# Performance work log

Measured on AMD Instinct MI355X. Metric: run time of the kernel, lower is better.

Reference implementation:

```python
import jax, jax.numpy as jnp
import numpy as np

# Config constants (repo-level globals)
N, S, P = 4096, 64, 64          # total peds, scenes, peds per scene (uniform)
H, E, MLPD, BOT = 64, 16, 64, 32  # h_dim, EMBEDDING_DIM, MLP_DIM, BOTTLENECK_DIM
PRED_LEN = 12
MIN_DIM = 3                      # mlp_input_dim = [rel_pos(2), speed(1)]
PP_HID = 512                     # hidden width of mlp_pre_pool


def setup_inputs() -> dict:
    key = jax.random.key(0)
    ks = jax.random.split(key, 24)
    sc = 0.1
    starts = jnp.arange(S, dtype=jnp.int32) * P
    inp = {
        "last_pos": jax.random.normal(ks[0], (N, 2), jnp.float32),
        "last_pos_rel": jax.random.normal(ks[1], (N, 2), jnp.float32),
        "h0": jax.random.normal(ks[2], (1, N, H), jnp.float32),
        "c0": jax.random.normal(ks[3], (1, N, H), jnp.float32),
        "pred_ped_speed": jax.random.uniform(ks[4], (PRED_LEN, N, 1), jnp.float32),
        # spatial_embedding: Linear(3, E)
        "W_sp": jax.random.normal(ks[5], (MIN_DIM, E)) * sc, "b_sp": jnp.zeros(E),
        # LSTM cell (torch gate order i,f,g,o)
        "W_ih": jax.random.normal(ks[6], (E, 4 * H)) * sc, "b_ih": jnp.zeros(4 * H),
        "W_hh": jax.random.normal(ks[7], (H, 4 * H)) * sc, "b_hh": jnp.zeros(4 * H),
        # hidden2pos: Linear(H, 2)
        "W_h2p": jax.random.normal(ks[8], (H, 2)) * sc, "b_h2p": jnp.zeros(2),
        # pooling pos_embedding: Linear(3, E)
        "W_pe": jax.random.normal(ks[9], (MIN_DIM, E)) * sc, "b_pe": jnp.zeros(E),
        # mlp_pre_pool: [E+H, 512, BOT], relu, no BN
        "W_pp1": jax.random.normal(ks[10], (E + H, PP_HID)) * sc, "b_pp1": jnp.zeros(PP_HID),
        "W_pp2": jax.random.normal(ks[11], (PP_HID, BOT)) * sc, "b_pp2": jnp.zeros(BOT),
        # decoder mlp: [H+BOT, MLPD, H], relu, no BN
        "W_m1": jax.random.normal(ks[12], (H + BOT, MLPD)) * sc, "b_m1": jnp.zeros(MLPD),
        "W_m2": jax.random.normal(ks[13], (MLPD, H)) * sc, "b_m2": jnp.zeros(H),
        "seq_start_end": jnp.stack([starts, starts + P], axis=1),
        "train_or_test": 0,
    }
    return inp


def reference(last_pos, last_pos_rel, h0, c0, pred_ped_speed,
              W_sp, b_sp, W_ih, b_ih, W_hh, b_hh, W_h2p, b_h2p,
              W_pe, b_pe, W_pp1, b_pp1, W_pp2, b_pp2,
              W_m1, b_m1, W_m2, b_m2, seq_start_end, train_or_test):
    relu = jax.nn.relu

    def lstm_cell(x, h, c):
        g = x @ W_ih + b_ih + h @ W_hh + b_hh
        i, f, gg, o = jnp.split(g, 4, axis=-1)
        c = jax.nn.sigmoid(f) * c + jax.nn.sigmoid(i) * jnp.tanh(gg)
        h = jax.nn.sigmoid(o) * jnp.tanh(c)
        return h, c

    def pool(h, pos, spd):
        # uniform scenes: reshape [N,*] -> [S,P,*]; pairwise index [s,i,j]
        hg = h.reshape(S, P, H)
        pg = pos.reshape(S, P, 2)
        sg = spd.reshape(S, P, 1)
        # social feature [s,i,j] = pos[j] - pos[i]  (curr_end_pos_1 - curr_end_pos_2)
        rel = pg[:, None, :, :] - pg[:, :, None, :]              # [S,P,P,2]
        feat = jnp.concatenate(
            [rel, jnp.broadcast_to(sg[:, None, :, :], (S, P, P, 1))], -1)  # speed of j
        emb = feat @ W_pe + b_pe                                  # [S,P,P,E]
        pre = jnp.concatenate(
            [jnp.broadcast_to(hg[:, None, :, :], (S, P, P, H)), emb], -1)  # h of j
        x = relu(pre @ W_pp1 + b_pp1)
        x = relu(x @ W_pp2 + b_pp2)                               # [S,P,P,BOT]
        return x.max(axis=2).reshape(-1, BOT)                     # max over j -> [N,BOT]

    # speed used at step id is pred_ped_speed[id+1], last step reuses final speed
    spd_seq = jnp.concatenate([pred_ped_speed[1:], pred_ped_speed[-1:]], axis=0)
    x0 = jnp.concatenate([last_pos_rel, pred_ped_speed[0]], -1) @ W_sp + b_sp

    def step(carry, spd_t):
        h, c, lp, x = carry
        h, c = lstm_cell(x, h, c)
        rel_pos = h @ W_h2p + b_h2p
        curr = rel_pos + lp
        x_new = jnp.concatenate([rel_pos, spd_t], -1) @ W_sp + b_sp
        pool_h = pool(h, curr, spd_t)
        h_new = relu(relu(jnp.concatenate([h, pool_h], -1) @ W_m1 + b_m1) @ W_m2 + b_m2)
        return (h_new, c, curr, x_new), rel_pos

    carry = (h0[0], c0[0], last_pos, x0)
    _, rels = jax.lax.scan(step, carry, spd_seq)
    return rels  # [PRED_LEN, N, 2]
```

## Files before the change

### kernel.cpp

```cpp
#include <hip/hip_runtime.h>

typedef unsigned int  u32;
typedef unsigned short u16;
typedef float  f32x4 __attribute__((ext_vector_type(4)));
typedef u32    u32x4 __attribute__((ext_vector_type(4)));
typedef __bf16 bf16x8 __attribute__((ext_vector_type(8)));
typedef _Float16 f16;
typedef _Float16 f16x8 __attribute__((ext_vector_type(8)));
typedef _Float16 f16x2 __attribute__((ext_vector_type(2)));

static constexpr int NPED = 4096;
static constexpr int H = 64, E = 16, BOT = 32, PPH = 512;
static constexpr int TSTEPS = 12;

__device__ __forceinline__ float bf2f(u16 u) {
  return __builtin_bit_cast(float, ((u32)u) << 16);
}
__device__ __forceinline__ u16 f2bf(float f) {
  u32 u = __builtin_bit_cast(u32, f);
  u += 0x7fffu + ((u >> 16) & 1u);
  return (u16)(u >> 16);
}
__device__ __forceinline__ u16 f2h(float f) {
  return __builtin_bit_cast(u16, (f16)f);
}
__device__ __forceinline__ float sigm(float x) { return 1.f / (1.f + __expf(-x)); }
__device__ __forceinline__ float tanhf_(float x) {
  float t = fabsf(x);
  float e = __expf(-2.f * t);
  float r = (1.f - e) / (1.f + e);
  return x < 0.f ? -r : r;
}
__device__ __forceinline__ f16x8 relu8(f16x8 t) {
  const f16x8 z = {(f16)0, (f16)0, (f16)0, (f16)0, (f16)0, (f16)0, (f16)0, (f16)0};
#if __has_builtin(__builtin_elementwise_max)
  return __builtin_elementwise_max(t, z);
#else
  #pragma unroll
  for (int q = 0; q < 8; ++q) t[q] = t[q] > (f16)0 ? t[q] : (f16)0;
  return t;
#endif
}

__device__ __forceinline__ void gload_lds16(const u16* __restrict__ g, u16* l) {
#if __has_builtin(__builtin_amdgcn_global_load_lds)
  __builtin_amdgcn_global_load_lds(
      (const __attribute__((address_space(1))) void*)g,
      (__attribute__((address_space(3))) void*)l, 16, 0, 0);
#else
  *(u32x4*)l = *(const u32x4*)g;
#endif
}

static constexpr size_t OFF_C    = 0;
static constexpr size_t OFF_HL   = 1048576;
static constexpr size_t OFF_POS  = 2097152;
static constexpr size_t OFF_X    = 2129920;
static constexpr size_t OFF_POOL = 2392064;
static constexpr size_t OFF_ABF  = 2916352;
static constexpr size_t OFF_A3   = 7110656;
static constexpr size_t OFF_CST  = 7116800;
static constexpr size_t OFF_W2T  = 7118848;
static constexpr size_t OFF_GWH  = 7151616;
static constexpr size_t OFF_GWL  = 7200768;
static constexpr size_t OFF_D1H  = 7249920;
static constexpr size_t OFF_D1L  = 7262208;
static constexpr size_t OFF_D2H  = 7274496;
static constexpr size_t OFF_D2L  = 7282688;
static constexpr size_t OFF_PWH  = 7290880;
static constexpr size_t OFF_PWL  = 7356416;
static constexpr size_t OFF_ABF2 = 7421952;
static constexpr size_t ABF_BYTES = (size_t)NPED * PPH * 2;
static constexpr size_t WS_NEED_FUSED = OFF_ABF2 + ABF_BYTES;

static constexpr int POOL_SMEM = 64*520*2 + 32*520*2 + 16*512*2 + 16*4*2*16*4;
static constexpr int FUSED_SMEM = POOL_SMEM + 64 + 128 + 128;

__global__ void k_setup(const float* __restrict__ last_pos, const float* __restrict__ last_pos_rel,
                        const float* __restrict__ c0, const float* __restrict__ pps,
                        const float* __restrict__ W_sp, const float* __restrict__ b_sp,
                        const float* __restrict__ W_pe, const float* __restrict__ b_pe,
                        const float* __restrict__ W_pp1, const float* __restrict__ b_pp1,
                        const float* __restrict__ W_pp2,
                        const float* __restrict__ W_ih, const float* __restrict__ W_hh,
                        const float* __restrict__ W_m1, const float* __restrict__ W_m2,
                        float* __restrict__ c, float* __restrict__ pos, float* __restrict__ x,
                        float* __restrict__ A3, float* __restrict__ Cst, u16* __restrict__ W2t,
                        u16* GWH, u16* GWL, u16* D1H, u16* D1L,
                        u16* D2H, u16* D2L, u16* PWH, u16* PWL)
{
  const int stride = gridDim.x * blockDim.x;
  const int tid0 = blockIdx.x * blockDim.x + threadIdx.x;
  for (int i = tid0; i < NPED * H; i += stride) c[i] = c0[i];
  for (int i = tid0; i < NPED * 2; i += stride) pos[i] = last_pos[i];
  for (int i = tid0; i < NPED * E; i += stride) {
    int n = i >> 4, e = i & 15;
    x[i] = last_pos_rel[2*n] * W_sp[e] + last_pos_rel[2*n+1] * W_sp[16+e]
         + pps[n] * W_sp[32+e] + b_sp[e];
  }
  for (int i = tid0; i < 3 * PPH; i += stride) {
    int r = i >> 9, k = i & 511;
    float s = 0.f;
    for (int e = 0; e < 16; ++e) s += W_pe[r*16+e] * W_pp1[(64+e)*PPH + k];
    A3[i] = s;
  }
  for (int i = tid0; i < PPH; i += stride) {
    float s = b_pp1[i];
    for (int e = 0; e < 16; ++e) s += b_pe[e] * W_pp1[(64+e)*PPH + i];
    Cst[i] = s;
  }
  for (int i = tid0; i < 32 * PPH; i += stride) {
    int n = i >> 9, k = i & 511;
    W2t[i] = f2h(W_pp2[k*32 + n]);
  }
  for (int i = tid0; i < 256*96; i += stride) {
    int n = i / 96, k = i - n*96;
    float wv = (k < 16) ? W_ih[k*256+n] : ((k < 80) ? W_hh[(k-16)*256+n] : 0.f);
    u16 hi = f2bf(wv); u16 lo = f2bf(wv - bf2f(hi));
    int idx = (((n>>4)*3 + (k>>5))*64 + ((k>>3)&3)*16 + (n&15))*8 + (k&7);
    GWH[idx] = hi; GWL[idx] = lo;
  }
  for (int i = tid0; i < 64*96; i += stride) {
    int n = i / 96, k = i - n*96;
    float wv = W_m1[k*64 + n];
    u16 hi = f2bf(wv); u16 lo = f2bf(wv - bf2f(hi));
    int idx = (((n>>4)*3 + (k>>5))*64 + ((k>>3)&3)*16 + (n&15))*8 + (k&7);
    D1H[idx] = hi; D1L[idx] = lo;
  }
  for (int i = tid0; i < 64*64; i += stride) {
    int n = i >> 6, k = i & 63;
    float wv = W_m2[k*64 + n];
    u16 hi = f2bf(wv); u16 lo = f2bf(wv - bf2f(hi));
    int idx = (((n>>4)*2 + (k>>5))*64 + ((k>>3)&3)*16 + (n&15))*8 + (k&7);
    D2H[idx] = hi; D2L[idx] = lo;
  }
  for (int i = tid0; i < 512*64; i += stride) {
    int n = i >> 6, k = i & 63;
    float wv = W_pp1[k*PPH + n];
    u16 hi = f2bf(wv); u16 lo = f2bf(wv - bf2f(hi));
    int idx = (((n>>4)*2 + (k>>5))*64 + ((k>>3)&3)*16 + (n&15))*8 + (k&7);
    PWH[idx] = hi; PWL[idx] = lo;
  }
}

template<int NT, int NKS>
__device__ __forceinline__ void load_frags(const u16* __restrict__ WH, const u16* __restrict__ WL,
                                           int tile0, int lane,
                                           u32x4 (&bh)[NT][NKS], u32x4 (&bl)[NT][NKS])
{
  #pragma unroll
  for (int i = 0; i < NT; ++i)
    #pragma unroll
    for (int ks = 0; ks < NKS; ++ks) {
      int o = (((tile0 + i)*NKS + ks)*64 + lane)*8;
      bh[i][ks] = *(const u32x4*)(WH + o);
      bl[i][ks] = *(const u32x4*)(WL + o);
    }
}

template<int NT, int NKS>
__device__ __forceinline__ void mfma_compute(const u32x4 (&bh)[NT][NKS], const u32x4 (&bl)[NT][NKS],
                                             int lane, const float* arow, f32x4* acc)
{
  const int kg = lane >> 4;
  #pragma unroll
  for (int ks = 0; ks < NKS; ++ks) {
    f32x4 a0 = *(const f32x4*)(arow + ks*32 + kg*8);
    f32x4 a1 = *(const f32x4*)(arow + ks*32 + kg*8 + 4);
    float av[8] = {a0.x,a0.y,a0.z,a0.w,a1.x,a1.y,a1.z,a1.w};
    bf16x8 ah, al;
    #pragma unroll
    for (int j = 0; j < 8; ++j) {
      __bf16 hbits = (__bf16)av[j];
      ah[j] = hbits;
      al[j] = (__bf16)(av[j] - (float)hbits);
    }
    #pragma unroll
    for (int i = 0; i < NT; ++i) {
      bf16x8 BH = __builtin_bit_cast(bf16x8, bh[i][ks]);
      bf16x8 BL = __builtin_bit_cast(bf16x8, bl[i][ks]);
      acc[i] = __builtin_amdgcn_mfma_f32_16x16x32_bf16(ah, BH, acc[i], 0, 0, 0);
      acc[i] = __builtin_amdgcn_mfma_f32_16x16x32_bf16(ah, BL, acc[i], 0, 0, 0);
      acc[i] = __builtin_amdgcn_mfma_f32_16x16x32_bf16(al, BH, acc[i], 0, 0, 0);
    }
  }
}

template<int NT, int NKS>
__device__ __forceinline__ void mfma_block(
    const u16* __restrict__ WH, const u16* __restrict__ WL, int tile0, int lane,
    const float* arow, int acol0, f32x4* acc)
{
  u32x4 bh[NT][NKS], bl[NT][NKS];
  load_frags<NT,NKS>(WH, WL, tile0, lane, bh, bl);
  mfma_compute<NT,NKS>(bh, bl, lane, arow + acol0, acc);
}

__global__ __launch_bounds__(256) void k_step(
    int t,
    const float* __restrict__ h0, const float* __restrict__ pps,
    float* __restrict__ c, float* __restrict__ h_lstm,
    float* __restrict__ pos, float* __restrict__ x, const float* __restrict__ pool,
    const float* __restrict__ b_ih, const float* __restrict__ b_hh,
    const float* __restrict__ W_h2p, const float* __restrict__ b_h2p,
    const float* __restrict__ W_sp, const float* __restrict__ b_sp,
    const float* __restrict__ b_m1, const float* __restrict__ b_m2,
    const float* __restrict__ A3, const float* __restrict__ Cst,
    const u16* __restrict__ GWH, const u16* __restrict__ GWL,
    const u16* __restrict__ D1H, const u16* __restrict__ D1L,
    const u16* __restrict__ D2H, const u16* __restrict__ D2L,
    const u16* __restrict__ PWH, const u16* __restrict__ PWL,
    u16* __restrict__ a_bf, float* __restrict__ out)
{
  __shared__ float zin[16][100];
  __shared__ float o1[16][68];
  __shared__ float as_[16][100];
  __shared__ float hl[16][68];
  __shared__ float gl[16][260];
  __shared__ float rel_s[16][2], pos_s[16][2], spd_s[16];

  const int tid = threadIdx.x;
  const int p0 = blockIdx.x * 16;
  const int w = tid >> 6, lane = tid & 63, colq = lane & 15, kg = lane >> 4;
  const int tsp = (t + 1 < 12) ? t + 1 : 11;

  { int p = tid >> 4, e = tid & 15;
    as_[p][e] = x[(p0 + p) * E + e];
    as_[p][80 + e] = 0.f; }
  if (tid < 16) spd_s[tid] = pps[tsp * NPED + p0 + tid];
  if (t == 0) {
    #pragma unroll
    for (int q = 0; q < 4; ++q) {
      int idx = tid + 256*q; int p = idx >> 6, d = idx & 63;
      as_[p][16 + d] = h0[(p0 + p) * H + d];
    }
  } else {
    #pragma unroll
    for (int q = 0; q < 4; ++q) {
      int idx = tid + 256*q; int p = idx >> 6, d = idx & 63;
      zin[p][d] = h_lstm[(p0 + p) * H + d];
    }
    #pragma unroll
    for (int q = 0; q < 2; ++q) {
      int idx = tid + 256*q; int p = idx >> 5, d = idx & 31;
      zin[p][64 + d] = pool[(p0 + p) * BOT + d];
    }
  }
  __syncthreads();

  if (t > 0) {
    {
      f32x4 acc = {0.f, 0.f, 0.f, 0.f};
      mfma_block<1,3>(D1H, D1L, w, lane, &zin[colq][0], 0, &acc);
      int n = w*16 + colq;
      float bm = b_m1[n];
      #pragma unroll
      for (int r = 0; r < 4; ++r) o1[kg*4 + r][n] = fmaxf(acc[r] + bm, 0.f);
    }
    __syncthreads();
    {
      f32x4 acc = {0.f, 0.f, 0.f, 0.f};
      mfma_block<1,2>(D2H, D2L, w, lane, &o1[colq][0], 0, &acc);
      int n = w*16 + colq;
      float bm = b_m2[n];
      #pragma unroll
      for (int r = 0; r < 4; ++r) as_[kg*4 + r][16 + n] = fmaxf(acc[r] + bm, 0.f);
    }
    __syncthreads();
  }

  {
    f32x4 gacc[4];
    #pragma unroll
    for (int i = 0; i < 4; ++i) gacc[i] = (f32x4){0.f,0.f,0.f,0.f};
    mfma_block<2,3>(GWH, GWL, w*4,     lane, &as_[colq][0], 0, &gacc[0]);
    mfma_block<2,3>(GWH, GWL, w*4 + 2, lane, &as_[colq][0], 0, &gacc[2]);
    #pragma unroll
    for (int i = 0; i < 4; ++i) {
      int n = (w*4 + i)*16 + colq;
      float bb = b_ih[n] + b_hh[n];
      #pragma unroll
      for (int r = 0; r < 4; ++r) gl[kg*4 + r][n] = gacc[i][r] + bb;
    }
  }
  __syncthreads();

  #pragma unroll
  for (int q = 0; q < 4; ++q) {
    int idx = tid + 256*q; int p = idx >> 6, d = idx & 63; int n = p0 + p;
    float gi = gl[p][d], gf = gl[p][64 + d], gg = gl[p][128 + d], go = gl[p][192 + d];
    float cv = c[n*H + d];
    float cn = sigm(gf) * cv + sigm(gi) * tanhf_(gg);
    float hv = sigm(go) * tanhf_(cn);
    c[n*H + d] = cn;
    hl[p][d] = hv;
    h_lstm[n*H + d] = hv;
  }
  __syncthreads();

  {
    int p = tid >> 4, l = tid & 15;
    f32x4 hv = *(const f32x4*)(&hl[p][0] + l*4);
    float s0 = hv.x * W_h2p[(l*4+0)*2]   + hv.y * W_h2p[(l*4+1)*2]
             + hv.z * W_h2p[(l*4+2)*2]   + hv.w * W_h2p[(l*4+3)*2];
    float s1 = hv.x * W_h2p[(l*4+0)*2+1] + hv.y * W_h2p[(l*4+1)*2+1]
             + hv.z * W_h2p[(l*4+2)*2+1] + hv.w * W_h2p[(l*4+3)*2+1];
    #pragma unroll
    for (int m = 1; m < 16; m <<= 1) {
      s0 += __shfl_xor(s0, m, 64);
      s1 += __shfl_xor(s1, m, 64);
    }
    if (l == 0) {
      float r0 = s0 + b_h2p[0], r1 = s1 + b_h2p[1];
      int n = p0 + p;
      float px = pos[n*2] + r0, py = pos[n*2+1] + r1;
      pos[n*2] = px; pos[n*2+1] = py;
      rel_s[p][0] = r0; rel_s[p][1] = r1;
      pos_s[p][0] = px; pos_s[p][1] = py;
      out[(t*NPED + n)*2] = r0; out[(t*NPED + n)*2 + 1] = r1;
    }
  }
  __syncthreads();

  if (t < 11) {
    {
      int p = tid >> 4, e = tid & 15;
      float xv = rel_s[p][0] * W_sp[e] + rel_s[p][1] * W_sp[16+e]
               + spd_s[p] * W_sp[32+e] + b_sp[e];
      x[(p0 + p) * E + e] = xv;
    }
    {
      f32x4 pacc[8];
      #pragma unroll
      for (int i = 0; i < 8; ++i) pacc[i] = (f32x4){0.f,0.f,0.f,0.f};
      mfma_block<4,2>(PWH, PWL, w*8,     lane, &hl[colq][0], 0, &pacc[0]);
      mfma_block<4,2>(PWH, PWL, w*8 + 4, lane, &hl[colq][0], 0, &pacc[4]);
      #pragma unroll
      for (int i = 0; i < 8; ++i) {
        int n = (w*8 + i)*16 + colq;
        float a3x = A3[n], a3y = A3[512 + n], a3s = A3[1024 + n], cst = Cst[n];
        #pragma unroll
        for (int r = 0; r < 4; ++r) {
          int p2 = kg*4 + r;
          float val = pacc[i][r] + pos_s[p2][0]*a3x + pos_s[p2][1]*a3y
                    + spd_s[p2]*a3s + cst;
          a_bf[(size_t)(p0 + p2)*PPH + n] = f2h(val);
        }
      }
    }
  }
}

__global__ __launch_bounds__(1024) void k_pool(
    const u16* __restrict__ a_bf, const float* __restrict__ pos,
    const float* __restrict__ A3, const u16* __restrict__ W2t,
    const float* __restrict__ b_pp2, float* __restrict__ pool)
{
  constexpr int LDA = 520;
  extern __shared__ char smem_raw[];
  u16* a_s  = (u16*)smem_raw;
  u16* w2_s = a_s + 64 * LDA;
  f16* v_s  = (f16*)(w2_s + 32 * LDA);
  float* red = (float*)(v_s + 16 * 512);

  const int tid = threadIdx.x;
  const int s = blockIdx.y;
  const int i0 = blockIdx.x * 16;

  for (int idx = tid; idx < 4096; idx += 1024) {
    int r = idx >> 6, c8 = (idx & 63) * 8;
    *(u32x4*)&a_s[r * LDA + c8] = *(const u32x4*)&a_bf[(s * 64 + r) * PPH + c8];
  }
  for (int idx = tid; idx < 2048; idx += 1024) {
    int r = idx >> 6, c8 = (idx & 63) * 8;
    *(u32x4*)&w2_s[r * LDA + c8] = *(const u32x4*)&W2t[r * PPH + c8];
  }
  for (int idx = tid; idx < 4096; idx += 1024) {
    int i = idx >> 8, k2 = (idx & 255) * 2;
    int n = s * 64 + i0 + i;
    float px = pos[n * 2], py = pos[n * 2 + 1];
    float v0 = px * A3[k2]     + py * A3[512 + k2];
    float v1 = px * A3[k2 + 1] + py * A3[512 + k2 + 1];
    f16x2 pk = { (f16)v0, (f16)v1 };
    *(f16x2*)&v_s[i * 512 + k2] = pk;
  }
  __syncthreads();

  const int lane = tid & 63, w = tid >> 6;
  const int jq = w & 3, g = w >> 2;
  const int col = lane & 15, kg = lane >> 4;
  const int aoff  = (jq * 16 + col) * LDA + kg * 8;
  const int w0off = col * LDA + kg * 8;
  const int w1off = (col + 16) * LDA + kg * 8;
  const float b20 = b_pp2[col];
  const float b21 = b_pp2[col + 16];
  const f32x4 vzero = {0.f, 0.f, 0.f, 0.f};

  f32x4 accA[4], accB[4];
  #pragma unroll
  for (int ii = 0; ii < 4; ++ii) { accA[ii] = vzero; accB[ii] = vzero; }

  for (int kk = 0; kk < 16; ++kk) {
    const int ke = kk * 32;
    f16x8 a8  = __builtin_bit_cast(f16x8, *(const u32x4*)&a_s[aoff + ke]);
    f16x8 bw0 = __builtin_bit_cast(f16x8, *(const u32x4*)&w2_s[w0off + ke]);
    f16x8 bw1 = __builtin_bit_cast(f16x8, *(const u32x4*)&w2_s[w1off + ke]);
    #pragma unroll
    for (int ii = 0; ii < 4; ++ii) {
      f16x8 v8 = *(const f16x8*)&v_s[(g * 4 + ii) * 512 + ke + kg * 8];
      f16x8 tq = relu8(a8 - v8);
      accA[ii] = __builtin_amdgcn_mfma_f32_16x16x32_f16(tq, bw0, accA[ii], 0, 0, 0);
      accB[ii] = __builtin_amdgcn_mfma_f32_16x16x32_f16(tq, bw1, accB[ii], 0, 0, 0);
    }
  }

  #pragma unroll
  for (int ii = 0; ii < 4; ++ii) {
    float m0 = 0.f, m1 = 0.f;
    #pragma unroll
    for (int r = 0; r < 4; ++r) {
      m0 = fmaxf(m0, accA[ii][r] + b20);
      m1 = fmaxf(m1, accB[ii][r] + b21);
    }
    m0 = fmaxf(m0, __shfl_xor(m0, 16, 64));
    m0 = fmaxf(m0, __shfl_xor(m0, 32, 64));
    m1 = fmaxf(m1, __shfl_xor(m1, 16, 64));
    m1 = fmaxf(m1, __shfl_xor(m1, 32, 64));
    if (kg == 0) {
      red[((w * 4 + ii) * 2 + 0) * 16 + col] = m0;
      red[((w * 4 + ii) * 2 + 1) * 16 + col] = m1;
    }
  }
  __syncthreads();

  if (tid < 512) {
    int gg = tid >> 7, ii = (tid >> 5) & 3, tile = (tid >> 4) & 1, cc = tid & 15;
    float m = red[(((gg * 4 + 0) * 4 + ii) * 2 + tile) * 16 + cc];
    #pragma unroll
    for (int q = 1; q < 4; ++q)
      m = fmaxf(m, red[(((gg * 4 + q) * 4 + ii) * 2 + tile) * 16 + cc]);
    int i = i0 + gg * 4 + ii;
    pool[(s * 64 + i) * 32 + tile * 16 + cc] = m;
  }
}

__global__ __launch_bounds__(1024) void k_fused(
    int t,
    const float* __restrict__ h0, const float* __restrict__ pps,
    float* __restrict__ c, float* __restrict__ h_lstm,
    float* __restrict__ pos, float* __restrict__ x,
    const float* __restrict__ b_ih, const float* __restrict__ b_hh,
    const float* __restrict__ W_h2p, const float* __restrict__ b_h2p,
    const float* __restrict__ W_sp, const float* __restrict__ b_sp,
    const float* __restrict__ b_m1, const float* __restrict__ b_m2,
    const float* __restrict__ A3, const float* __restrict__ Cst,
    const u16* __restrict__ GWH, const u16* __restrict__ GWL,
    const u16* __restrict__ D1H, const u16* __restrict__ D1L,
    const u16* __restrict__ D2H, const u16* __restrict__ D2L,
    const u16* __restrict__ PWH, const u16* __restrict__ PWL,
    const u16* __restrict__ W2t, const float* __restrict__ b_pp2,
    const u16* __restrict__ a_read, u16* __restrict__ a_write,
    float* __restrict__ out)
{
  constexpr int LDA = 520;
  extern __shared__ char smem_raw[];
  u16*   a_s    = (u16*)smem_raw;
  u16*   w2_s   = a_s + 64 * LDA;
  f16*   v_s    = (f16*)(w2_s + 32 * LDA);
  float* red    = (float*)(v_s + 16 * 512);
  float* spd_s  = red + 16*4*2*16;
  float* rel_s  = spd_s + 16;
  float* pos_s  = rel_s + 32;
  float* zin = (float*)smem_raw;
  float* o1  = zin + 16*100;
  float* as_ = o1  + 16*68;
  float* hl  = as_ + 16*100;
  float* gl  = hl  + 16*68;

  const int tid = threadIdx.x;
  const int s = blockIdx.y;
  const int i0 = blockIdx.x * 16;
  const int p0 = s * 64 + i0;
  const int lane = tid & 63, w = tid >> 6;
  const int colq = lane & 15, kg = lane >> 4;
  const int sd = tid & 63;
  const int tsp = (t + 1 < 12) ? t + 1 : 11;

  const float* hsrc = (t == 0) ? h0 : h_lstm;
  float hreg = hsrc[(p0 + w) * H + sd];
  float creg = c[(p0 + w) * H + sd];
  float whp0 = W_h2p[2 * sd], whp1 = W_h2p[2 * sd + 1];
  float xreg = 0.f;
  if (tid < 256) xreg = x[(p0 + (tid >> 4)) * E + (tid & 15)];
  if (tid < 16) spd_s[tid] = pps[tsp * NPED + p0 + tid];

  u32x4 gh[1][3], glo[1][3];
  u32x4 d1h_[1][3], d1l_[1][3], d2h_[1][2], d2l_[1][2];

  if (t > 0) {
    #pragma unroll
    for (int q = 0; q < 4; ++q) {
      int r = w + 16 * q;
      gload_lds16(&a_read[(size_t)(s * 64 + r) * PPH + lane * 8],
                  &a_s[r * LDA + lane * 8]);
    }
    #pragma unroll
    for (int q = 0; q < 2; ++q) {
      int r = w + 16 * q;
      gload_lds16(&W2t[(size_t)r * PPH + lane * 8],
                  &w2_s[r * LDA + lane * 8]);
    }
    for (int idx = tid; idx < 4096; idx += 1024) {
      int i = idx >> 8, k2 = (idx & 255) * 2;
      int n = s * 64 + i0 + i;
      float px = pos[n * 2], py = pos[n * 2 + 1];
      float v0 = px * A3[k2]     + py * A3[512 + k2];
      float v1 = px * A3[k2 + 1] + py * A3[512 + k2 + 1];
      f16x2 pk = { (f16)v0, (f16)v1 };
      *(f16x2*)&v_s[i * 512 + k2] = pk;
    }
    __syncthreads();

    {
      const int jq = w & 3, g = w >> 2;
      const int aoff  = (jq * 16 + colq) * LDA + kg * 8;
      const int w0off = colq * LDA + kg * 8;
      const int w1off = (colq + 16) * LDA + kg * 8;
      const float b20 = b_pp2[colq];
      const float b21 = b_pp2[colq + 16];
      const f32x4 vzero = {0.f, 0.f, 0.f, 0.f};

      f32x4 accA[4], accB[4];
      #pragma unroll
      for (int ii = 0; ii < 4; ++ii) { accA[ii] = vzero; accB[ii] = vzero; }

      for (int kk = 0; kk < 16; ++kk) {
        const int ke = kk * 32;
        f16x8 a8  = __builtin_bit_cast(f16x8, *(const u32x4*)&a_s[aoff + ke]);
        f16x8 bw0 = __builtin_bit_cast(f16x8, *(const u32x4*)&w2_s[w0off + ke]);
        f16x8 bw1 = __builtin_bit_cast(f16x8, *(const u32x4*)&w2_s[w1off + ke]);
        #pragma unroll
        for (int ii = 0; ii < 4; ++ii) {
          f16x8 v8 = *(const f16x8*)&v_s[(g * 4 + ii) * 512 + ke + kg * 8];
          f16x8 tq = relu8(a8 - v8);
          accA[ii] = __builtin_amdgcn_mfma_f32_16x16x32_f16(tq, bw0, accA[ii], 0, 0, 0);
          accB[ii] = __builtin_amdgcn_mfma_f32_16x16x32_f16(tq, bw1, accB[ii], 0, 0, 0);
        }
      }

      #pragma unroll
      for (int ii = 0; ii < 4; ++ii) {
        float m0 = 0.f, m1 = 0.f;
        #pragma unroll
        for (int r = 0; r < 4; ++r) {
          m0 = fmaxf(m0, accA[ii][r] + b20);
          m1 = fmaxf(m1, accB[ii][r] + b21);
        }
        m0 = fmaxf(m0, __shfl_xor(m0, 16, 64));
        m0 = fmaxf(m0, __shfl_xor(m0, 32, 64));
        m1 = fmaxf(m1, __shfl_xor(m1, 16, 64));
        m1 = fmaxf(m1, __shfl_xor(m1, 32, 64));
        if (kg == 0) {
          red[((w * 4 + ii) * 2 + 0) * 16 + colq] = m0;
          red[((w * 4 + ii) * 2 + 1) * 16 + colq] = m1;
        }
      }
    }
    load_frags<1,3>(GWH, GWL, w, lane, gh, glo);
    if (w < 4) {
      load_frags<1,3>(D1H, D1L, w, lane, d1h_, d1l_);
      load_frags<1,2>(D2H, D2L, w, lane, d2h_, d2l_);
    }
    __syncthreads();

    zin[w * 100 + sd] = hreg;
    if (tid < 512) {
      int gg = tid >> 7, ii = (tid >> 5) & 3, tile = (tid >> 4) & 1, cc = tid & 15;
      float m = red[(((gg * 4 + 0) * 4 + ii) * 2 + tile) * 16 + cc];
      #pragma unroll
      for (int q = 1; q < 4; ++q)
        m = fmaxf(m, red[(((gg * 4 + q) * 4 + ii) * 2 + tile) * 16 + cc]);
      zin[(gg * 4 + ii) * 100 + 64 + tile * 16 + cc] = m;
    }
    if (tid < 256) { int p = tid >> 4, e = tid & 15;
                     as_[p * 100 + e] = xreg; as_[p * 100 + 80 + e] = 0.f; }
    __syncthreads();

    if (w < 4) {
      f32x4 acc = {0.f, 0.f, 0.f, 0.f};
      mfma_compute<1,3>(d1h_, d1l_, lane, &zin[colq * 100], &acc);
      int n = w * 16 + colq;
      float bm = b_m1[n];
      #pragma unroll
      for (int r = 0; r < 4; ++r) o1[(kg * 4 + r) * 68 + n] = fmaxf(acc[r] + bm, 0.f);
    }
    __syncthreads();

    if (w < 4) {
      f32x4 acc = {0.f, 0.f, 0.f, 0.f};
      mfma_compute<1,2>(d2h_, d2l_, lane, &o1[colq * 68], &acc);
      int n = w * 16 + colq;
      float bm = b_m2[n];
      #pragma unroll
      for (int r = 0; r < 4; ++r) as_[(kg * 4 + r) * 100 + 16 + n] = fmaxf(acc[r] + bm, 0.f);
    }
    __syncthreads();
  } else {
    load_frags<1,3>(GWH, GWL, w, lane, gh, glo);
    as_[w * 100 + 16 + sd] = hreg;
    if (tid < 256) { int p = tid >> 4, e = tid & 15;
                     as_[p * 100 + e] = xreg; as_[p * 100 + 80 + e] = 0.f; }
    __syncthreads();
  }

  {
    f32x4 acc = {0.f, 0.f, 0.f, 0.f};
    mfma_compute<1,3>(gh, glo, lane, &as_[colq * 100], &acc);
    int n = w * 16 + colq;
    float bb = b_ih[n] + b_hh[n];
    #pragma unroll
    for (int r = 0; r < 4; ++r) gl[(kg * 4 + r) * 260 + n] = acc[r] + bb;
  }
  u32x4 ph[2][2], pl[2][2];
  if (t < 11) load_frags<2,2>(PWH, PWL, w * 2, lane, ph, pl);
  __syncthreads();

  {
    int n = p0 + w;
    float gi = gl[w*260 + sd], gf = gl[w*260 + 64 + sd],
          gg = gl[w*260 + 128 + sd], go = gl[w*260 + 192 + sd];
    float cn = sigm(gf) * creg + sigm(gi) * tanhf_(gg);
    float hv = sigm(go) * tanhf_(cn);
    c[n*H + sd] = cn;
    hl[w*68 + sd] = hv;
    h_lstm[n*H + sd] = hv;
    float s0 = hv * whp0, s1 = hv * whp1;
    #pragma unroll
    for (int m = 1; m < 64; m <<= 1) {
      s0 += __shfl_xor(s0, m, 64);
      s1 += __shfl_xor(s1, m, 64);
    }
    if (sd == 0) {
      float r0 = s0 + b_h2p[0], r1 = s1 + b_h2p[1];
      float px = pos[n*2] + r0, py = pos[n*2+1] + r1;
      pos[n*2] = px; pos[n*2+1] = py;
      rel_s[w*2+0] = r0; rel_s[w*2+1] = r1;
      pos_s[w*2+0] = px; pos_s[w*2+1] = py;
      out[(t*NPED + n)*2] = r0; out[(t*NPED + n)*2 + 1] = r1;
    }
  }
  __syncthreads();

  if (t < 11) {
    if (tid < 256) {
      int p = tid >> 4, e = tid & 15;
      float xv = rel_s[p*2+0] * W_sp[e] + rel_s[p*2+1] * W_sp[16+e]
               + spd_s[p] * W_sp[32+e] + b_sp[e];
      x[(p0 + p) * E + e] = xv;
    }
    {
      f32x4 pacc[2];
      pacc[0] = (f32x4){0.f,0.f,0.f,0.f};
      pacc[1] = (f32x4){0.f,0.f,0.f,0.f};
      mfma_compute<2,2>(ph, pl, lane, &hl[colq * 68], pacc);
      #pragma unroll
      for (int i = 0; i < 2; ++i) {
        int n = (w * 2 + i) * 16 + colq;
        float a3x = A3[n], a3y = A3[512 + n], a3s = A3[1024 + n], cst = Cst[n];
        #pragma unroll
        for (int r = 0; r < 4; ++r) {
          int p2 = kg * 4 + r;
          float val = pacc[i][r] + pos_s[p2*2+0]*a3x + pos_s[p2*2+1]*a3y
                    + spd_s[p2]*a3s + cst;
          a_write[(size_t)(p0 + p2) * PPH + n] = f2h(val);
        }
      }
    }
  }
}

extern "C" void kernel_launch(void* const* d_in, const int* in_sizes, int n_in,
                              void* d_out, int out_size, void* d_ws, size_t ws_size,
                              hipStream_t stream)
{
  const float* last_pos     = (const float*)d_in[0];
  const float* last_pos_rel = (const float*)d_in[1];
  const float* h0    = (const float*)d_in[2];
  const float* c0    = (const float*)d_in[3];
  const float* pps   = (const float*)d_in[4];
  const float* W_sp  = (const float*)d_in[5];
  const float* b_sp  = (const float*)d_in[6];
  const float* W_ih  = (const float*)d_in[7];
  const float* b_ih  = (const float*)d_in[8];
  const float* W_hh  = (const float*)d_in[9];
  const float* b_hh  = (const float*)d_in[10];
  const float* W_h2p = (const float*)d_in[11];
  const float* b_h2p = (const float*)d_in[12];
  const float* W_pe  = (const float*)d_in[13];
  const float* b_pe  = (const float*)d_in[14];
  const float* W_pp1 = (const float*)d_in[15];
  const float* b_pp1 = (const float*)d_in[16];
  const float* W_pp2 = (const float*)d_in[17];
  const float* b_pp2 = (const float*)d_in[18];
  const float* W_m1  = (const float*)d_in[19];
  const float* b_m1  = (const float*)d_in[20];
  const float* W_m2  = (const float*)d_in[21];
  const float* b_m2  = (const float*)d_in[22];

  char* ws = (char*)d_ws;
  float* c_buf  = (float*)(ws + OFF_C);
  float* h_lstm = (float*)(ws + OFF_HL);
  float* pos    = (float*)(ws + OFF_POS);
  float* x_buf  = (float*)(ws + OFF_X);
  float* pool   = (float*)(ws + OFF_POOL);
  u16*   abuf0  = (u16*)(ws + OFF_ABF);
  float* A3     = (float*)(ws + OFF_A3);
  float* Cst    = (float*)(ws + OFF_CST);
  u16*   W2t    = (u16*)(ws + OFF_W2T);
  u16* GWH = (u16*)(ws + OFF_GWH); u16* GWL = (u16*)(ws + OFF_GWL);
  u16* D1H = (u16*)(ws + OFF_D1H); u16* D1L = (u16*)(ws + OFF_D1L);
  u16* D2H = (u16*)(ws + OFF_D2H); u16* D2L = (u16*)(ws + OFF_D2L);
  u16* PWH = (u16*)(ws + OFF_PWH); u16* PWL = (u16*)(ws + OFF_PWL);
  u16*   abuf1  = (u16*)(ws + OFF_ABF2);
  float* out    = (float*)d_out;

  const bool fused_ok = (ws_size >= WS_NEED_FUSED);

  hipFuncSetAttribute(reinterpret_cast<const void*>(k_pool),
                      hipFuncAttributeMaxDynamicSharedMemorySize, POOL_SMEM);
  hipFuncSetAttribute(reinterpret_cast<const void*>(k_fused),
                      hipFuncAttributeMaxDynamicSharedMemorySize, FUSED_SMEM);

  k_setup<<<512, 256, 0, stream>>>(last_pos, last_pos_rel, c0, pps, W_sp, b_sp,
                                   W_pe, b_pe, W_pp1, b_pp1, W_pp2,
                                   W_ih, W_hh, W_m1, W_m2,
                                   c_buf, pos, x_buf, A3, Cst, W2t,
                                   GWH, GWL, D1H, D1L, D2H, D2L, PWH, PWL);

  if (fused_ok) {
    for (int t = 0; t < TSTEPS; ++t) {
      const u16* ar = (t > 0 && ((t - 1) & 1)) ? abuf1 : abuf0;
      u16*       aw = (t & 1) ? abuf1 : abuf0;
      k_fused<<<dim3(4, 64), 1024, FUSED_SMEM, stream>>>(
          t, h0, pps, c_buf, h_lstm, pos, x_buf,
          b_ih, b_hh, W_h2p, b_h2p, W_sp, b_sp, b_m1, b_m2, A3, Cst,
          GWH, GWL, D1H, D1L, D2H, D2L, PWH, PWL,
          W2t, b_pp2, ar, aw, out);
    }
  } else {
    k_step<<<256, 256, 0, stream>>>(0, h0, pps, c_buf, h_lstm, pos, x_buf, pool,
                                    b_ih, b_hh, W_h2p, b_h2p, W_sp, b_sp,
                                    b_m1, b_m2, A3, Cst,
                                    GWH, GWL, D1H, D1L, D2H, D2L, PWH, PWL,
                                    abuf0, out);
    for (int t = 1; t < TSTEPS; ++t) {
      k_pool<<<dim3(4, 64), 1024, POOL_SMEM, stream>>>(abuf0, pos, A3, W2t, b_pp2, pool);
      k_step<<<256, 256, 0, stream>>>(t, h0, pps, c_buf, h_lstm, pos, x_buf, pool,
                                      b_ih, b_hh, W_h2p, b_h2p, W_sp, b_sp,
                                      b_m1, b_m2, A3, Cst,
                                      GWH, GWL, D1H, D1L, D2H, D2L, PWH, PWL,
                                      abuf0, out);
    }
  }
}
```

Before: 266.6 us.

## Replace per-step fused launches with one persistent per-scene kernel

Replaces the twelve per-timestep k_fused launches (256 blocks of 16 peds) with a single persistent k_pers kernel where each of 64 blocks owns a whole scene of 64 peds across all timesteps. It keeps h, c, x and positions in registers and shared memory, which removes the global round-trips and the double-buffered pre-pool activation buffer. Since a scene is self-contained, no grid sync is needed. In exchange only 64 blocks run, so each block processes four times as many pool rows sequentially and far fewer CUs are used.

```diff
diff --git a/kernel.cpp b/kernel.cpp
--- a/kernel.cpp
+++ b/kernel.cpp
@@ -72,9 +72,12 @@
 static constexpr size_t OFF_ABF2 = 7421952;
 static constexpr size_t ABF_BYTES = (size_t)NPED * PPH * 2;
 static constexpr size_t WS_NEED_FUSED = OFF_ABF2 + ABF_BYTES;
+static constexpr size_t WS_NEED_PERS  = OFF_ABF + ABF_BYTES;
 
 static constexpr int POOL_SMEM = 64*520*2 + 32*520*2 + 16*512*2 + 16*4*2*16*4;
 static constexpr int FUSED_SMEM = POOL_SMEM + 64 + 128 + 128;
+static constexpr int PERS_UNION = 152576;
+static constexpr int PERS_SMEM  = PERS_UNION + 64*32*4 + 64*4 + 64*2*4 + 64*2*4;
 
 __global__ void k_setup(const float* __restrict__ last_pos, const float* __restrict__ last_pos_rel,
                         const float* __restrict__ c0, const float* __restrict__ pps,
@@ -194,6 +197,278 @@
   u32x4 bh[NT][NKS], bl[NT][NKS];
   load_frags<NT,NKS>(WH, WL, tile0, lane, bh, bl);
   mfma_compute<NT,NKS>(bh, bl, lane, arow + acol0, acc);
+}
+
+__global__ __launch_bounds__(1024) void k_pers(
+    const float* __restrict__ h0, const float* __restrict__ c0,
+    const float* __restrict__ pps,
+    const float* __restrict__ last_pos, const float* __restrict__ x_g,
+    const float* __restrict__ b_ih, const float* __restrict__ b_hh,
+    const float* __restrict__ W_h2p, const float* __restrict__ b_h2p,
+    const float* __restrict__ W_sp, const float* __restrict__ b_sp,
+    const float* __restrict__ b_m1, const float* __restrict__ b_m2,
+    const float* __restrict__ A3, const float* __restrict__ Cst,
+    const u16* __restrict__ GWH, const u16* __restrict__ GWL,
+    const u16* __restrict__ D1H, const u16* __restrict__ D1L,
+    const u16* __restrict__ D2H, const u16* __restrict__ D2L,
+    const u16* __restrict__ PWH, const u16* __restrict__ PWL,
+    const u16* __restrict__ W2t, const float* __restrict__ b_pp2,
+    u16* __restrict__ a_g, float* __restrict__ out)
+{
+  constexpr int LDA = 520;
+  extern __shared__ char smem[];
+  u16*   a_s  = (u16*)smem;
+  u16*   w2_s = a_s + 64 * LDA;
+  f16*   v_s  = (f16*)(w2_s + 32 * LDA);
+  float* red  = (float*)(v_s + 16 * 512);
+  float* zin = (float*)smem;
+  float* o1  = zin + 64*100;
+  float* as_ = o1  + 64*68;
+  float* hl  = as_ + 64*100;
+  float* gl  = hl  + 64*68;
+  float* pool_out = (float*)(smem + PERS_UNION);
+  float* spd_s    = pool_out + 64*32;
+  float* rel_s    = spd_s + 64;
+  float* pos_s    = rel_s + 128;
+
+  const int tid = threadIdx.x;
+  const int base = blockIdx.x * 64;
+  const int lane = tid & 63, w = tid >> 6;
+  const int colq = lane & 15, kg = lane >> 4;
+  const int sd = lane;
+
+  float creg[4], hreg[4];
+  #pragma unroll
+  for (int q = 0; q < 4; ++q) {
+    int p = w + 16*q;
+    creg[q] = c0[(base + p)*H + sd];
+    hreg[q] = h0[(base + p)*H + sd];
+  }
+  float xreg = x_g[(base + (tid >> 4))*E + (tid & 15)];
+  const float whp0 = W_h2p[2*sd], whp1 = W_h2p[2*sd + 1];
+  if (tid < 64) {
+    pos_s[tid*2+0] = last_pos[(base + tid)*2+0];
+    pos_s[tid*2+1] = last_pos[(base + tid)*2+1];
+  }
+  __syncthreads();
+
+  for (int t = 0; t < TSTEPS; ++t) {
+    const int tsp = (t + 1 < 12) ? t + 1 : 11;
+    if (tid < 64) spd_s[tid] = pps[tsp * NPED + base + tid];
+
+    if (t > 0) {
+      #pragma unroll
+      for (int q = 0; q < 4; ++q) {
+        int r = w + 16*q;
+        gload_lds16(&a_g[(size_t)(base + r)*PPH + lane*8], &a_s[r*LDA + lane*8]);
+      }
+      #pragma unroll
+      for (int q = 0; q < 2; ++q) {
+        int r = w + 16*q;
+        gload_lds16(&W2t[(size_t)r*PPH + lane*8], &w2_s[r*LDA + lane*8]);
+      }
+
+      const int jq = w & 3, g2 = w >> 2;
+      const int aoff  = (jq*16 + colq)*LDA + kg*8;
+      const int w0off = colq*LDA + kg*8;
+      const int w1off = (colq + 16)*LDA + kg*8;
+      const float b20 = b_pp2[colq];
+      const float b21 = b_pp2[colq + 16];
+
+      for (int gg = 0; gg < 4; ++gg) {
+        for (int idx = tid; idx < 4096; idx += 1024) {
+          int il = idx >> 8, k2 = (idx & 255)*2;
+          int i = gg*16 + il;
+          float px = pos_s[i*2], py = pos_s[i*2+1];
+          float v0 = px*A3[k2]     + py*A3[512 + k2];
+          float v1 = px*A3[k2+1]   + py*A3[512 + k2 + 1];
+          f16x2 pk = { (f16)v0, (f16)v1 };
+          *(f16x2*)&v_s[il*512 + k2] = pk;
+        }
+        if (gg > 0 && tid < 512) {
+          int g3 = tid >> 7, ii = (tid >> 5) & 3, tile = (tid >> 4) & 1, cc = tid & 15;
+          float m = red[(((g3*4 + 0)*4 + ii)*2 + tile)*16 + cc];
+          #pragma unroll
+          for (int q = 1; q < 4; ++q)
+            m = fmaxf(m, red[(((g3*4 + q)*4 + ii)*2 + tile)*16 + cc]);
+          pool_out[((gg-1)*16 + g3*4 + ii)*32 + tile*16 + cc] = m;
+        }
+        __syncthreads();
+
+        f32x4 accA[4], accB[4];
+        #pragma unroll
+        for (int ii = 0; ii < 4; ++ii) {
+          accA[ii] = (f32x4){0.f,0.f,0.f,0.f};
+          accB[ii] = (f32x4){0.f,0.f,0.f,0.f};
+        }
+        for (int kk = 0; kk < 16; ++kk) {
+          const int ke = kk * 32;
+          f16x8 a8  = __builtin_bit_cast(f16x8, *(const u32x4*)&a_s[aoff + ke]);
+          f16x8 bw0 = __builtin_bit_cast(f16x8, *(const u32x4*)&w2_s[w0off + ke]);
+          f16x8 bw1 = __builtin_bit_cast(f16x8, *(const u32x4*)&w2_s[w1off + ke]);
+          #pragma unroll
+          for (int ii = 0; ii < 4; ++ii) {
+            f16x8 v8 = *(const f16x8*)&v_s[(g2*4 + ii)*512 + ke + kg*8];
+            f16x8 tq = relu8(a8 - v8);
+            accA[ii] = __builtin_amdgcn_mfma_f32_16x16x32_f16(tq, bw0, accA[ii], 0, 0, 0);
+            accB[ii] = __builtin_amdgcn_mfma_f32_16x16x32_f16(tq, bw1, accB[ii], 0, 0, 0);
+          }
+        }
+        #pragma unroll
+        for (int ii = 0; ii < 4; ++ii) {
+          float m0 = 0.f, m1 = 0.f;
+          #pragma unroll
+          for (int r = 0; r < 4; ++r) {
+            m0 = fmaxf(m0, accA[ii][r] + b20);
+            m1 = fmaxf(m1, accB[ii][r] + b21);
+          }
+          m0 = fmaxf(m0, __shfl_xor(m0, 16, 64));
+          m0 = fmaxf(m0, __shfl_xor(m0, 32, 64));
+          m1 = fmaxf(m1, __shfl_xor(m1, 16, 64));
+          m1 = fmaxf(m1, __shfl_xor(m1, 32, 64));
+          if (kg == 0) {
+            red[((w*4 + ii)*2 + 0)*16 + colq] = m0;
+            red[((w*4 + ii)*2 + 1)*16 + colq] = m1;
+          }
+        }
+        __syncthreads();
+      }
+
+      #pragma unroll
+      for (int q = 0; q < 4; ++q) zin[(w + 16*q)*100 + sd] = hreg[q];
+      if (tid < 512) {
+        int g3 = tid >> 7, ii = (tid >> 5) & 3, tile = (tid >> 4) & 1, cc = tid & 15;
+        float m = red[(((g3*4 + 0)*4 + ii)*2 + tile)*16 + cc];
+        #pragma unroll
+        for (int q = 1; q < 4; ++q)
+          m = fmaxf(m, red[(((g3*4 + q)*4 + ii)*2 + tile)*16 + cc]);
+        pool_out[(48 + g3*4 + ii)*32 + tile*16 + cc] = m;
+      }
+      { int p = tid >> 4, e = tid & 15;
+        as_[p*100 + e] = xreg; as_[p*100 + 80 + e] = 0.f; }
+      __syncthreads();
+      for (int idx = tid; idx < 2048; idx += 1024) {
+        int i = idx >> 5, j = idx & 31;
+        zin[i*100 + 64 + j] = pool_out[i*32 + j];
+      }
+      __syncthreads();
+
+      {
+        const int mt = w >> 2, nt = w & 3;
+        f32x4 acc = {0.f, 0.f, 0.f, 0.f};
+        u32x4 dh[1][3], dl[1][3];
+        load_frags<1,3>(D1H, D1L, nt, lane, dh, dl);
+        mfma_compute<1,3>(dh, dl, lane, &zin[(mt*16 + colq)*100], &acc);
+        int n = nt*16 + colq;
+        float bm = b_m1[n];
+        #pragma unroll
+        for (int r = 0; r < 4; ++r)
+          o1[(mt*16 + kg*4 + r)*68 + n] = fmaxf(acc[r] + bm, 0.f);
+      }
+      __syncthreads();
+
+      {
+        const int mt = w >> 2, nt = w & 3;
+        f32x4 acc = {0.f, 0.f, 0.f, 0.f};
+        u32x4 dh[1][2], dl[1][2];
+        load_frags<1,2>(D2H, D2L, nt, lane, dh, dl);
+        mfma_compute<1,2>(dh, dl, lane, &o1[(mt*16 + colq)*68], &acc);
+        int n = nt*16 + colq;
+        float bm = b_m2[n];
+        #pragma unroll
+        for (int r = 0; r < 4; ++r)
+          as_[(mt*16 + kg*4 + r)*100 + 16 + n] = fmaxf(acc[r] + bm, 0.f);
+      }
+      __syncthreads();
+    } else {
+      #pragma unroll
+      for (int q = 0; q < 4; ++q) as_[(w + 16*q)*100 + 16 + sd] = hreg[q];
+      { int p = tid >> 4, e = tid & 15;
+        as_[p*100 + e] = xreg; as_[p*100 + 80 + e] = 0.f; }
+      __syncthreads();
+    }
+
+    {
+      u32x4 gh[1][3], glo[1][3];
+      load_frags<1,3>(GWH, GWL, w, lane, gh, glo);
+      const int n = w*16 + colq;
+      const float bb = b_ih[n] + b_hh[n];
+      #pragma unroll
+      for (int mt = 0; mt < 4; ++mt) {
+        f32x4 acc = {0.f, 0.f, 0.f, 0.f};
+        mfma_compute<1,3>(gh, glo, lane, &as_[(mt*16 + colq)*100], &acc);
+        #pragma unroll
+        for (int r = 0; r < 4; ++r)
+          gl[(mt*16 + kg*4 + r)*260 + n] = acc[r] + bb;
+      }
+    }
+    __syncthreads();
+
+    {
+      float hv4[4];
+      #pragma unroll
+      for (int q = 0; q < 4; ++q) {
+        int p = w + 16*q;
+        float gi = gl[p*260 + sd], gf = gl[p*260 + 64 + sd],
+              gg = gl[p*260 + 128 + sd], go = gl[p*260 + 192 + sd];
+        float cn = sigm(gf)*creg[q] + sigm(gi)*tanhf_(gg);
+        float hv = sigm(go)*tanhf_(cn);
+        creg[q] = cn; hreg[q] = hv; hv4[q] = hv;
+        hl[p*68 + sd] = hv;
+      }
+      #pragma unroll
+      for (int q = 0; q < 4; ++q) {
+        float s0 = hv4[q]*whp0, s1 = hv4[q]*whp1;
+        #pragma unroll
+        for (int m = 1; m < 64; m <<= 1) {
+          s0 += __shfl_xor(s0, m, 64);
+          s1 += __shfl_xor(s1, m, 64);
+        }
+        if (sd == 0) {
+          int p = w + 16*q;
+          float r0 = s0 + b_h2p[0], r1 = s1 + b_h2p[1];
+          float px = pos_s[p*2+0] + r0, py = pos_s[p*2+1] + r1;
+          pos_s[p*2+0] = px; pos_s[p*2+1] = py;
+          rel_s[p*2+0] = r0; rel_s[p*2+1] = r1;
+          int n = base + p;
+          out[(t*NPED + n)*2] = r0; out[(t*NPED + n)*2 + 1] = r1;
+        }
+      }
+    }
+    __syncthreads();
+
+    if (t < 11) {
+      {
+        int p = tid >> 4, e = tid & 15;
+        xreg = rel_s[p*2+0]*W_sp[e] + rel_s[p*2+1]*W_sp[16+e]
+             + spd_s[p]*W_sp[32+e] + b_sp[e];
+      }
+      {
+        u32x4 ph[2][2], pl[2][2];
+        load_frags<2,2>(PWH, PWL, w*2, lane, ph, pl);
+        #pragma unroll
+        for (int mt = 0; mt < 4; ++mt) {
+          f32x4 pacc[2];
+          pacc[0] = (f32x4){0.f,0.f,0.f,0.f};
+          pacc[1] = (f32x4){0.f,0.f,0.f,0.f};
+          mfma_compute<2,2>(ph, pl, lane, &hl[(mt*16 + colq)*68], pacc);
+          #pragma unroll
+          for (int i = 0; i < 2; ++i) {
+            int n = (w*2 + i)*16 + colq;
+            float a3x = A3[n], a3y = A3[512 + n], a3s = A3[1024 + n], cst = Cst[n];
+            #pragma unroll
+            for (int r = 0; r < 4; ++r) {
+              int p2 = mt*16 + kg*4 + r;
+              float val = pacc[i][r] + pos_s[p2*2+0]*a3x + pos_s[p2*2+1]*a3y
+                        + spd_s[p2]*a3s + cst;
+              a_g[(size_t)(base + p2)*PPH + n] = f2h(val);
+            }
+          }
+        }
+      }
+    }
+    __syncthreads();
+  }
 }
 
 __global__ __launch_bounds__(256) void k_step(
@@ -441,241 +716,6 @@
       m = fmaxf(m, red[(((gg * 4 + q) * 4 + ii) * 2 + tile) * 16 + cc]);
     int i = i0 + gg * 4 + ii;
     pool[(s * 64 + i) * 32 + tile * 16 + cc] = m;
-  }
-}
-
-__global__ __launch_bounds__(1024) void k_fused(
-    int t,
-    const float* __restrict__ h0, const float* __restrict__ pps,
-    float* __restrict__ c, float* __restrict__ h_lstm,
-    float* __restrict__ pos, float* __restrict__ x,
-    const float* __restrict__ b_ih, const float* __restrict__ b_hh,
-    const float* __restrict__ W_h2p, const float* __restrict__ b_h2p,
-    const float* __restrict__ W_sp, const float* __restrict__ b_sp,
-    const float* __restrict__ b_m1, const float* __restrict__ b_m2,
-    const float* __restrict__ A3, const float* __restrict__ Cst,
-    const u16* __restrict__ GWH, const u16* __restrict__ GWL,
-    const u16* __restrict__ D1H, const u16* __restrict__ D1L,
-    const u16* __restrict__ D2H, const u16* __restrict__ D2L,
-    const u16* __restrict__ PWH, const u16* __restrict__ PWL,
-    const u16* __restrict__ W2t, const float* __restrict__ b_pp2,
-    const u16* __restrict__ a_read, u16* __restrict__ a_write,
-    float* __restrict__ out)
-{
-  constexpr int LDA = 520;
-  extern __shared__ char smem_raw[];
-  u16*   a_s    = (u16*)smem_raw;
-  u16*   w2_s   = a_s + 64 * LDA;
-  f16*   v_s    = (f16*)(w2_s + 32 * LDA);
-  float* red    = (float*)(v_s + 16 * 512);
-  float* spd_s  = red + 16*4*2*16;
-  float* rel_s  = spd_s + 16;
-  float* pos_s  = rel_s + 32;
-  float* zin = (float*)smem_raw;
-  float* o1  = zin + 16*100;
-  float* as_ = o1  + 16*68;
-  float* hl  = as_ + 16*100;
-  float* gl  = hl  + 16*68;
-
-  const int tid = threadIdx.x;
-  const int s = blockIdx.y;
-  const int i0 = blockIdx.x * 16;
-  const int p0 = s * 64 + i0;
-  const int lane = tid & 63, w = tid >> 6;
-  const int colq = lane & 15, kg = lane >> 4;
-  const int sd = tid & 63;
-  const int tsp = (t + 1 < 12) ? t + 1 : 11;
-
-  const float* hsrc = (t == 0) ? h0 : h_lstm;
-  float hreg = hsrc[(p0 + w) * H + sd];
-  float creg = c[(p0 + w) * H + sd];
-  float whp0 = W_h2p[2 * sd], whp1 = W_h2p[2 * sd + 1];
-  float xreg = 0.f;
-  if (tid < 256) xreg = x[(p0 + (tid >> 4)) * E + (tid & 15)];
-  if (tid < 16) spd_s[tid] = pps[tsp * NPED + p0 + tid];
-
-  u32x4 gh[1][3], glo[1][3];
-  u32x4 d1h_[1][3], d1l_[1][3], d2h_[1][2], d2l_[1][2];
-
-  if (t > 0) {
-    #pragma unroll
-    for (int q = 0; q < 4; ++q) {
-      int r = w + 16 * q;
-      gload_lds16(&a_read[(size_t)(s * 64 + r) * PPH + lane * 8],
-                  &a_s[r * LDA + lane * 8]);
-    }
-    #pragma unroll
-    for (int q = 0; q < 2; ++q) {
-      int r = w + 16 * q;
-      gload_lds16(&W2t[(size_t)r * PPH + lane * 8],
-                  &w2_s[r * LDA + lane * 8]);
-    }
-    for (int idx = tid; idx < 4096; idx += 1024) {
-      int i = idx >> 8, k2 = (idx & 255) * 2;
-      int n = s * 64 + i0 + i;
-      float px = pos[n * 2], py = pos[n * 2 + 1];
-      float v0 = px * A3[k2]     + py * A3[512 + k2];
-      float v1 = px * A3[k2 + 1] + py * A3[512 + k2 + 1];
-      f16x2 pk = { (f16)v0, (f16)v1 };
-      *(f16x2*)&v_s[i * 512 + k2] = pk;
-    }
-    __syncthreads();
-
-    {
-      const int jq = w & 3, g = w >> 2;
-      const int aoff  = (jq * 16 + colq) * LDA + kg * 8;
-      const int w0off = colq * LDA + kg * 8;
-      const int w1off = (colq + 16) * LDA + kg * 8;
-      const float b20 = b_pp2[colq];
-      const float b21 = b_pp2[colq + 16];
-      const f32x4 vzero = {0.f, 0.f, 0.f, 0.f};
-
-      f32x4 accA[4], accB[4];
-      #pragma unroll
-      for (int ii = 0; ii < 4; ++ii) { accA[ii] = vzero; accB[ii] = vzero; }
-
-      for (int kk = 0; kk < 16; ++kk) {
-        const int ke = kk * 32;
-        f16x8 a8  = __builtin_bit_cast(f16x8, *(const u32x4*)&a_s[aoff + ke]);
-        f16x8 bw0 = __builtin_bit_cast(f16x8, *(const u32x4*)&w2_s[w0off + ke]);
-        f16x8 bw1 = __builtin_bit_cast(f16x8, *(const u32x4*)&w2_s[w1off + ke]);
-        #pragma unroll
-        for (int ii = 0; ii < 4; ++ii) {
-          f16x8 v8 = *(const f16x8*)&v_s[(g * 4 + ii) * 512 + ke + kg * 8];
-          f16x8 tq = relu8(a8 - v8);
-          accA[ii] = __builtin_amdgcn_mfma_f32_16x16x32_f16(tq, bw0, accA[ii], 0, 0, 0);
-          accB[ii] = __builtin_amdgcn_mfma_f32_16x16x32_f16(tq, bw1, accB[ii], 0, 0, 0);
-        }
-      }
-
-      #pragma unroll
-      for (int ii = 0; ii < 4; ++ii) {
-        float m0 = 0.f, m1 = 0.f;
-        #pragma unroll
-        for (int r = 0; r < 4; ++r) {
-          m0 = fmaxf(m0, accA[ii][r] + b20);
-          m1 = fmaxf(m1, accB[ii][r] + b21);
-        }
-        m0 = fmaxf(m0, __shfl_xor(m0, 16, 64));
-        m0 = fmaxf(m0, __shfl_xor(m0, 32, 64));
-        m1 = fmaxf(m1, __shfl_xor(m1, 16, 64));
-        m1 = fmaxf(m1, __shfl_xor(m1, 32, 64));
-        if (kg == 0) {
-          red[((w * 4 + ii) * 2 + 0) * 16 + colq] = m0;
-          red[((w * 4 + ii) * 2 + 1) * 16 + colq] = m1;
-        }
-      }
-    }
-    load_frags<1,3>(GWH, GWL, w, lane, gh, glo);
-    if (w < 4) {
-      load_frags<1,3>(D1H, D1L, w, lane, d1h_, d1l_);
-      load_frags<1,2>(D2H, D2L, w, lane, d2h_, d2l_);
-    }
-    __syncthreads();
-
-    zin[w * 100 + sd] = hreg;
-    if (tid < 512) {
-      int gg = tid >> 7, ii = (tid >> 5) & 3, tile = (tid >> 4) & 1, cc = tid & 15;
-      float m = red[(((gg * 4 + 0) * 4 + ii) * 2 + tile) * 16 + cc];
-      #pragma unroll
-      for (int q = 1; q < 4; ++q)
-        m = fmaxf(m, red[(((gg * 4 + q) * 4 + ii) * 2 + tile) * 16 + cc]);
-      zin[(gg * 4 + ii) * 100 + 64 + tile * 16 + cc] = m;
-    }
-    if (tid < 256) { int p = tid >> 4, e = tid & 15;
-                     as_[p * 100 + e] = xreg; as_[p * 100 + 80 + e] = 0.f; }
-    __syncthreads();
-
-    if (w < 4) {
-      f32x4 acc = {0.f, 0.f, 0.f, 0.f};
-      mfma_compute<1,3>(d1h_, d1l_, lane, &zin[colq * 100], &acc);
-      int n = w * 16 + colq;
-      float bm = b_m1[n];
-      #pragma unroll
-      for (int r = 0; r < 4; ++r) o1[(kg * 4 + r) * 68 + n] = fmaxf(acc[r] + bm, 0.f);
-    }
-    __syncthreads();
-
-    if (w < 4) {
-      f32x4 acc = {0.f, 0.f, 0.f, 0.f};
-      mfma_compute<1,2>(d2h_, d2l_, lane, &o1[colq * 68], &acc);
-      int n = w * 16 + colq;
-      float bm = b_m2[n];
-      #pragma unroll
-      for (int r = 0; r < 4; ++r) as_[(kg * 4 + r) * 100 + 16 + n] = fmaxf(acc[r] + bm, 0.f);
-    }
-    __syncthreads();
-  } else {
-    load_frags<1,3>(GWH, GWL, w, lane, gh, glo);
-    as_[w * 100 + 16 + sd] = hreg;
-    if (tid < 256) { int p = tid >> 4, e = tid & 15;
-                     as_[p * 100 + e] = xreg; as_[p * 100 + 80 + e] = 0.f; }
-    __syncthreads();
-  }
-
-  {
-    f32x4 acc = {0.f, 0.f, 0.f, 0.f};
-    mfma_compute<1,3>(gh, glo, lane, &as_[colq * 100], &acc);
-    int n = w * 16 + colq;
-    float bb = b_ih[n] + b_hh[n];
-    #pragma unroll
-    for (int r = 0; r < 4; ++r) gl[(kg * 4 + r) * 260 + n] = acc[r] + bb;
-  }
-  u32x4 ph[2][2], pl[2][2];
-  if (t < 11) load_frags<2,2>(PWH, PWL, w * 2, lane, ph, pl);
-  __syncthreads();
-
-  {
-    int n = p0 + w;
-    float gi = gl[w*260 + sd], gf = gl[w*260 + 64 + sd],
-          gg = gl[w*260 + 128 + sd], go = gl[w*260 + 192 + sd];
-    float cn = sigm(gf) * creg + sigm(gi) * tanhf_(gg);
-    float hv = sigm(go) * tanhf_(cn);
-    c[n*H + sd] = cn;
-    hl[w*68 + sd] = hv;
-    h_lstm[n*H + sd] = hv;
-    float s0 = hv * whp0, s1 = hv * whp1;
-    #pragma unroll
-    for (int m = 1; m < 64; m <<= 1) {
-      s0 += __shfl_xor(s0, m, 64);
-      s1 += __shfl_xor(s1, m, 64);
-    }
-    if (sd == 0) {
-      float r0 = s0 + b_h2p[0], r1 = s1 + b_h2p[1];
-      float px = pos[n*2] + r0, py = pos[n*2+1] + r1;
-      pos[n*2] = px; pos[n*2+1] = py;
-      rel_s[w*2+0] = r0; rel_s[w*2+1] = r1;
-      pos_s[w*2+0] = px; pos_s[w*2+1] = py;
-      out[(t*NPED + n)*2] = r0; out[(t*NPED + n)*2 + 1] = r1;
-    }
-  }
-  __syncthreads();
-
-  if (t < 11) {
-    if (tid < 256) {
-      int p = tid >> 4, e = tid & 15;
-      float xv = rel_s[p*2+0] * W_sp[e] + rel_s[p*2+1] * W_sp[16+e]
-               + spd_s[p] * W_sp[32+e] + b_sp[e];
-      x[(p0 + p) * E + e] = xv;
-    }
-    {
-      f32x4 pacc[2];
-      pacc[0] = (f32x4){0.f,0.f,0.f,0.f};
-      pacc[1] = (f32x4){0.f,0.f,0.f,0.f};
-      mfma_compute<2,2>(ph, pl, lane, &hl[colq * 68], pacc);
-      #pragma unroll
-      for (int i = 0; i < 2; ++i) {
-        int n = (w * 2 + i) * 16 + colq;
-        float a3x = A3[n], a3y = A3[512 + n], a3s = A3[1024 + n], cst = Cst[n];
-        #pragma unroll
-        for (int r = 0; r < 4; ++r) {
-          int p2 = kg * 4 + r;
-          float val = pacc[i][r] + pos_s[p2*2+0]*a3x + pos_s[p2*2+1]*a3y
-                    + spd_s[p2]*a3s + cst;
-          a_write[(size_t)(p0 + p2) * PPH + n] = f2h(val);
-        }
-      }
-    }
   }
 }
 
@@ -721,15 +761,14 @@
   u16* D1H = (u16*)(ws + OFF_D1H); u16* D1L = (u16*)(ws + OFF_D1L);
   u16* D2H = (u16*)(ws + OFF_D2H); u16* D2L = (u16*)(ws + OFF_D2L);
   u16* PWH = (u16*)(ws + OFF_PWH); u16* PWL = (u16*)(ws + OFF_PWL);
-  u16*   abuf1  = (u16*)(ws + OFF_ABF2);
   float* out    = (float*)d_out;
 
-  const bool fused_ok = (ws_size >= WS_NEED_FUSED);
-
-  hipFuncSetAttribute(reinterpret_cast<const void*>(k_pool),
-                      hipFuncAttributeMaxDynamicSharedMemorySize, POOL_SMEM);
-  hipFuncSetAttribute(reinterpret_cast<const void*>(k_fused),
-                      hipFuncAttributeMaxDynamicSharedMemorySize, FUSED_SMEM);
+  static int pers_ok = -1;
+  if (pers_ok < 0) {
+    hipError_t e = hipFuncSetAttribute(reinterpret_cast<const void*>(k_pers),
+                                       hipFuncAttributeMaxDynamicSharedMemorySize, PERS_SMEM);
+    pers_ok = (e == hipSuccess) ? 1 : 0;
+  }
 
   k_setup<<<512, 256, 0, stream>>>(last_pos, last_pos_rel, c0, pps, W_sp, b_sp,
                                    W_pe, b_pe, W_pp1, b_pp1, W_pp2,
@@ -737,17 +776,15 @@
                                    c_buf, pos, x_buf, A3, Cst, W2t,
                                    GWH, GWL, D1H, D1L, D2H, D2L, PWH, PWL);
 
-  if (fused_ok) {
-    for (int t = 0; t < TSTEPS; ++t) {
-      const u16* ar = (t > 0 && ((t - 1) & 1)) ? abuf1 : abuf0;
-      u16*       aw = (t & 1) ? abuf1 : abuf0;
-      k_fused<<<dim3(4, 64), 1024, FUSED_SMEM, stream>>>(
-          t, h0, pps, c_buf, h_lstm, pos, x_buf,
-          b_ih, b_hh, W_h2p, b_h2p, W_sp, b_sp, b_m1, b_m2, A3, Cst,
-          GWH, GWL, D1H, D1L, D2H, D2L, PWH, PWL,
-          W2t, b_pp2, ar, aw, out);
-    }
+  if (pers_ok && ws_size >= WS_NEED_PERS) {
+    k_pers<<<64, 1024, PERS_SMEM, stream>>>(
+        h0, c0, pps, last_pos, x_buf,
+        b_ih, b_hh, W_h2p, b_h2p, W_sp, b_sp, b_m1, b_m2, A3, Cst,
+        GWH, GWL, D1H, D1L, D2H, D2L, PWH, PWL,
+        W2t, b_pp2, abuf0, out);
   } else {
+    hipFuncSetAttribute(reinterpret_cast<const void*>(k_pool),
+                        hipFuncAttributeMaxDynamicSharedMemorySize, POOL_SMEM);
     k_step<<<256, 256, 0, stream>>>(0, h0, pps, c_buf, h_lstm, pos, x_buf, pool,
                                     b_ih, b_hh, W_h2p, b_h2p, W_sp, b_sp,
                                     b_m1, b_m2, A3, Cst,
```

New measurement: 954.0 us. +257.9%, slower.
